# Kernel optimization log

Measured on AMD Instinct MI355X. Metric: run time of the kernel, lower is better.

## Reference

```python
import jax, jax.numpy as jnp
import numpy as np

BAG, SEQ, D = 8, 512, 768      # docs per bag, seq len, bert hidden (d_model)
NB = 4                          # bridge spans kept per doc (subsampling cap regime)
NPD = 2 + NB                    # nodes per doc: h, t, bridges
N = BAG * NPD                   # total entity nodes in the bag graph (48)
T = N * N                       # matrix cells fed to MatTransformer (2304)
H = 8
DK = D // H                     # head dim 96
DFF, L = 1024, 4                # MatTransformer ffn width / num_layers
NREL = 97                       # num_relations (DocRED)
EPS = 1e-5


def _ln(x, g, b):
    m = jnp.mean(x, axis=-1, keepdims=True)
    v = jnp.var(x, axis=-1, keepdims=True)
    return (x - m) * jax.lax.rsqrt(v + EPS) * g + b


def setup_inputs() -> dict:
    key = jax.random.key(0)
    ks = jax.random.split(key, 16)
    s = 0.02
    p = {}
    # stand-in for BERT last hidden states
    p['embedding'] = jax.random.normal(ks[0], (BAG, SEQ, D), jnp.float32)
    # entity spans per doc: [h, t, b1..bNB] x (start, end) inclusive, from get_htb markers
    starts = jax.random.randint(ks[1], (BAG, NPD), 0, SEQ - 9)
    lens = jax.random.randint(ks[2], (BAG, NPD), 1, 9)
    p['spans'] = jnp.stack([starts, starts + lens - 1], axis=-1).astype(jnp.int32)
    # pairwise relation encoders wu / wv / ln1
    p['Wu'] = jax.random.normal(ks[3], (D, D)) * s; p['bu'] = jnp.zeros((D,))
    p['Wv'] = jax.random.normal(ks[4], (D, D)) * s; p['bv'] = jnp.zeros((D,))
    p['Wl'] = jax.random.normal(ks[5], (D, D)) * s; p['bl'] = jnp.zeros((D,))
    # MatTransformer: L layers of MHA + FFN, params stacked over layers
    p['Wq'] = jax.random.normal(ks[6], (L, D, D)) * s;  p['bq'] = jnp.zeros((L, D))
    p['Wk'] = jax.random.normal(ks[7], (L, D, D)) * s;  p['bk'] = jnp.zeros((L, D))
    p['Wvm'] = jax.random.normal(ks[8], (L, D, D)) * s; p['bvm'] = jnp.zeros((L, D))
    p['Wo'] = jax.random.normal(ks[9], (L, D, D)) * s;  p['bo'] = jnp.zeros((L, D))
    p['F1'] = jax.random.normal(ks[10], (L, D, DFF)) * s; p['f1'] = jnp.zeros((L, DFF))
    p['F2'] = jax.random.normal(ks[11], (L, DFF, D)) * s; p['f2'] = jnp.zeros((L, D))
    p['g1'] = jnp.ones((L, D)); p['be1'] = jnp.zeros((L, D))
    p['g2'] = jnp.ones((L, D)); p['be2'] = jnp.zeros((L, D))
    # final norm + predictor
    p['ng'] = jnp.ones((D,)); p['nb'] = jnp.zeros((D,))
    p['Wp'] = jax.random.normal(ks[12], (D, NREL)) * s; p['bp'] = jnp.zeros((NREL,))
    return p


def _forward(embedding, spans, Wu, bu, Wv, bv, Wl, bl, Wq, bq, Wk, bk, Wvm, bvm,
             Wo, bo, F1, f1, F2, f2, g1, be1, g2, be2, ng, nb, Wp, bp):
    # --- ragged span gather + max pooling (masked max, vectorized) ---
    pos = jnp.arange(SEQ)
    m = (pos >= spans[..., :1]) & (pos <= spans[..., 1:])          # [BAG, NPD, SEQ]
    neg = jnp.finfo(embedding.dtype).min
    pooled = jnp.max(jnp.where(m[..., None], embedding[:, None, :, :], neg), axis=2)  # [BAG, NPD, D]
    htb = pooled.reshape(N, D)                                      # h/t/bridge node embs
    # --- pairwise outer-sum relation encoding: relu(ln1(relu(u_i + v_j))) ---
    u = htb @ Wu + bu
    v = htb @ Wv + bv
    rel = jax.nn.relu(jax.nn.relu(u[:, None, :] + v[None, :, :]) @ Wl + bl)  # [N, N, D]
    # --- MatTransformer: multi-head self-attention over the N*N matrix cells ---
    x = rel.reshape(T, D)
    scale = 1.0 / np.sqrt(DK).astype(np.float32)
    for l in range(L):
        q = (x @ Wq[l] + bq[l]).reshape(T, H, DK)
        k = (x @ Wk[l] + bk[l]).reshape(T, H, DK)
        vv = (x @ Wvm[l] + bvm[l]).reshape(T, H, DK)
        att = jax.nn.softmax(jnp.einsum('qhd,khd->hqk', q, k) * scale, axis=-1)
        o = jnp.einsum('hqk,khd->qhd', att, vv).reshape(T, D) @ Wo[l] + bo[l]
        x = _ln(x + o, g1[l], be1[l])
        f = jax.nn.relu(x @ F1[l] + f1[l]) @ F2[l] + f2[l]
        x = _ln(x + f, g2[l], be2[l])
    rel_m = x.reshape(N, N, D)
    # --- gather (h_pos, t_pos) cells: h at i*NPD, t at i*NPD+1 ---
    hp = jnp.arange(BAG) * NPD
    t_feature = rel_m[hp, hp + 1]                                   # [BAG, D]
    ht_logits = _ln(t_feature, ng, nb) @ Wp + bp                    # [BAG, NREL]
    bag_logit = jnp.max(ht_logits, axis=0, keepdims=True)           # [1, NREL]
    return bag_logit, ht_logits


def reference(embedding, spans, Wu, bu, Wv, bv, Wl, bl, Wq, bq, Wk, bk, Wvm, bvm,
              Wo, bo, F1, f1, F2, f2, g1, be1, g2, be2, ng, nb, Wp, bp):
    return _forward(embedding, spans, Wu, bu, Wv, bv, Wl, bl, Wq, bq, Wk, bk,
                    Wvm, bvm, Wo, bo, F1, f1, F2, f2, g1, be1, g2, be2, ng, nb, Wp, bp)
```

## Files before the change

kernel.cpp:

```cpp
#include <hip/hip_runtime.h>
#include <hip/hip_bf16.h>

typedef __hip_bfloat16 bf16;
typedef __bf16 bf16x8 __attribute__((ext_vector_type(8)));
typedef float f32x4 __attribute__((ext_vector_type(4)));

#define BAG 8
#define SEQ 512
#define DM 768
#define NPD 6
#define NNODE 48
#define TT 2304
#define NH 8
#define DKH 96
#define DFF 1024
#define NLAYER 4
#define NREL 97
#define SP 6
#define KSPAN (TT / SP)
#define LN_EPS 1e-5f

__device__ __forceinline__ float b2f(const bf16 x) { return __bfloat162float(x); }
__device__ __forceinline__ bf16 f2b(float f) { return __float2bfloat16(f); }
__device__ __forceinline__ unsigned short f2bu(float f) {
    bf16 h = __float2bfloat16(f);
    return *reinterpret_cast<unsigned short*>(&h);
}

__global__ __launch_bounds__(256) void span_pool(const float* __restrict__ emb,
                                                 const int* __restrict__ spans,
                                                 bf16* __restrict__ htb) {
    const int n = blockIdx.x;
    const int b = n / NPD;
    int s0 = spans[n * 2 + 0];
    int s1 = spans[n * 2 + 1];
    s0 = min(max(s0, 0), SEQ - 1);
    s1 = min(max(s1, s0), SEQ - 1);
    const float* base = emb + (size_t)b * SEQ * DM;
    for (int d = threadIdx.x; d < DM; d += 256) {
        float m = -3.0e38f;
        for (int s = s0; s <= s1; ++s) m = fmaxf(m, base[(size_t)s * DM + d]);
        htb[(size_t)n * DM + d] = f2b(m);
    }
}

__global__ __launch_bounds__(256) void prep_wt3(const float* __restrict__ W0,
                                                const float* __restrict__ W1,
                                                const float* __restrict__ W2,
                                                bf16* __restrict__ Wt) {
    __shared__ __align__(16) __bf16 tile[64][72];
    const int z = blockIdx.z;
    const float* W = (z == 0) ? W0 : (z == 1) ? W1 : W2;
    bf16* out = Wt + (size_t)z * DM * DM;
    const int t = threadIdx.x;
    const int k0 = blockIdx.x * 64, n0 = blockIdx.y * 64;
    const int r = t >> 2, cg = (t & 3) * 16;
#pragma unroll
    for (int i = 0; i < 4; ++i) {
        const float4 v = *(const float4*)&W[(size_t)(k0 + r) * DM + n0 + cg + 4 * i];
        tile[r][cg + 4 * i + 0] = (__bf16)v.x;
        tile[r][cg + 4 * i + 1] = (__bf16)v.y;
        tile[r][cg + 4 * i + 2] = (__bf16)v.z;
        tile[r][cg + 4 * i + 3] = (__bf16)v.w;
    }
    __syncthreads();
#pragma unroll
    for (int i = 0; i < 2; ++i) {
        bf16x8 o;
#pragma unroll
        for (int j = 0; j < 8; ++j) o[j] = tile[cg + 8 * i + j][r];
        *(bf16x8*)&out[(size_t)(n0 + r) * DM + k0 + cg + 8 * i] = o;
    }
}

__global__ __launch_bounds__(256) void prep6(const float* __restrict__ Wq,
                                             const float* __restrict__ Wk,
                                             const float* __restrict__ Wv,
                                             const float* __restrict__ Wo,
                                             const float* __restrict__ F1,
                                             const float* __restrict__ F2,
                                             bf16* __restrict__ slab) {
    __shared__ __align__(16) __bf16 tile[64][72];
    const int z = blockIdx.z;
    int K = DM, N = DM;
    const float* W;
    size_t off;
    switch (z) {
        case 0: W = Wq; off = 0;       break;
        case 1: W = Wk; off = 589824;  break;
        case 2: W = Wv; off = 1179648; break;
        case 3: W = Wo; off = 1769472; break;
        case 4: W = F1; off = 2359296; N = DFF; break;
        default: W = F2; off = 3145728; K = DFF; break;
    }
    const int k0 = blockIdx.x * 64, n0 = blockIdx.y * 64;
    if (k0 >= K || n0 >= N) return;
    bf16* out = slab + off;
    const int t = threadIdx.x;
    const int r = t >> 2, cg = (t & 3) * 16;
#pragma unroll
    for (int i = 0; i < 4; ++i) {
        const float4 v = *(const float4*)&W[(size_t)(k0 + r) * N + n0 + cg + 4 * i];
        tile[r][cg + 4 * i + 0] = (__bf16)v.x;
        tile[r][cg + 4 * i + 1] = (__bf16)v.y;
        tile[r][cg + 4 * i + 2] = (__bf16)v.z;
        tile[r][cg + 4 * i + 3] = (__bf16)v.w;
    }
    __syncthreads();
#pragma unroll
    for (int i = 0; i < 2; ++i) {
        bf16x8 o;
#pragma unroll
        for (int j = 0; j < 8; ++j) o[j] = tile[cg + 8 * i + j][r];
        *(bf16x8*)&out[(size_t)(n0 + r) * K + k0 + cg + 8 * i] = o;
    }
}

template <int RELU, int DUAL>
__global__ __launch_bounds__(256) void gemm_bt256(const bf16* __restrict__ A,
                                                  const bf16* __restrict__ Bt,
                                                  const float* __restrict__ bias,
                                                  const float* __restrict__ bias2,
                                                  bf16* __restrict__ C,
                                                  int M, int N, int K) {
    __shared__ __align__(16) __bf16 As[2][64][72];
    __shared__ __align__(16) __bf16 Bs[2][64][72];
    const int t = threadIdx.x;
    const int w = t >> 6, lane = t & 63;
    const int quad = lane >> 4, l15 = lane & 15;
    const int wr = w >> 1, wc = w & 1;
    const int row0 = blockIdx.y * 64, col0 = blockIdx.x * 64;
    const int s_row = t >> 2, s_off = (t & 3) * 16;
    const bool a_ok = (row0 + s_row) < M;

    const f32x4 fz = {0.f, 0.f, 0.f, 0.f};
    f32x4 acc[2][2];
#pragma unroll
    for (int m = 0; m < 2; ++m)
#pragma unroll
        for (int n = 0; n < 2; ++n) acc[m][n] = fz;

    bf16x8 av[2], bv[2];
#pragma unroll
    for (int j = 0; j < 2; ++j)
#pragma unroll
        for (int e = 0; e < 8; ++e) av[j][e] = (__bf16)0.0f;
    if (a_ok)
#pragma unroll
        for (int j = 0; j < 2; ++j)
            av[j] = *(const bf16x8*)&A[(size_t)(row0 + s_row) * K + s_off + 8 * j];
#pragma unroll
    for (int j = 0; j < 2; ++j)
        bv[j] = *(const bf16x8*)&Bt[(size_t)(col0 + s_row) * K + s_off + 8 * j];

    int cur = 0;
    for (int k0 = 0; k0 < K; k0 += 64) {
#pragma unroll
        for (int j = 0; j < 2; ++j) {
            *(bf16x8*)&As[cur][s_row][s_off + 8 * j] = av[j];
            *(bf16x8*)&Bs[cur][s_row][s_off + 8 * j] = bv[j];
        }
        __syncthreads();

        if (k0 + 64 < K) {
            if (a_ok)
#pragma unroll
                for (int j = 0; j < 2; ++j)
                    av[j] = *(const bf16x8*)&A[(size_t)(row0 + s_row) * K + k0 + 64 + s_off + 8 * j];
#pragma unroll
            for (int j = 0; j < 2; ++j)
                bv[j] = *(const bf16x8*)&Bt[(size_t)(col0 + s_row) * K + k0 + 64 + s_off + 8 * j];
        }

#pragma unroll
        for (int kk = 0; kk < 2; ++kk) {
            const bf16x8 af0 = *(const bf16x8*)&As[cur][wr * 32 + l15][quad * 8 + 32 * kk];
            const bf16x8 af1 = *(const bf16x8*)&As[cur][wr * 32 + 16 + l15][quad * 8 + 32 * kk];
            const bf16x8 bf0 = *(const bf16x8*)&Bs[cur][wc * 32 + l15][quad * 8 + 32 * kk];
            const bf16x8 bf1 = *(const bf16x8*)&Bs[cur][wc * 32 + 16 + l15][quad * 8 + 32 * kk];
            acc[0][0] = __builtin_amdgcn_mfma_f32_16x16x32_bf16(af0, bf0, acc[0][0], 0, 0, 0);
            acc[0][1] = __builtin_amdgcn_mfma_f32_16x16x32_bf16(af0, bf1, acc[0][1], 0, 0, 0);
            acc[1][0] = __builtin_amdgcn_mfma_f32_16x16x32_bf16(af1, bf0, acc[1][0], 0, 0, 0);
            acc[1][1] = __builtin_amdgcn_mfma_f32_16x16x32_bf16(af1, bf1, acc[1][1], 0, 0, 0);
        }
        cur ^= 1;
    }

#pragma unroll
    for (int n = 0; n < 2; ++n) {
        const int col = col0 + wc * 32 + 16 * n + l15;
        const float bvl = (DUAL && col >= DM) ? bias2[col - DM] : bias[col];
#pragma unroll
        for (int m = 0; m < 2; ++m)
#pragma unroll
            for (int r = 0; r < 4; ++r) {
                const int row = row0 + wr * 32 + 16 * m + quad * 4 + r;
                if (row < M) {
                    float v = acc[m][n][r] + bvl;
                    if (RELU) v = fmaxf(v, 0.f);
                    C[(size_t)row * N + col] = f2b(v);
                }
            }
    }
}

__global__ __launch_bounds__(256) void gemm_qkv256(const bf16* __restrict__ A,
                                                   const bf16* __restrict__ Bt,
                                                   const float* __restrict__ b0,
                                                   const float* __restrict__ b1,
                                                   const float* __restrict__ b2,
                                                   bf16* __restrict__ C0,
                                                   bf16* __restrict__ C1,
                                                   bf16* __restrict__ Vt) {
    __shared__ __align__(16) __bf16 As[2][64][72];
    __shared__ __align__(16) __bf16 Bs[2][64][72];
    const int t = threadIdx.x;
    const int w = t >> 6, lane = t & 63;
    const int quad = lane >> 4, l15 = lane & 15;
    const int wr = w >> 1, wc = w & 1;
    const int row0 = blockIdx.y * 64, col0 = blockIdx.x * 64;
    const int s_row = t >> 2, s_off = (t & 3) * 16;

    const f32x4 fz = {0.f, 0.f, 0.f, 0.f};
    f32x4 acc[2][2];
#pragma unroll
    for (int m = 0; m < 2; ++m)
#pragma unroll
        for (int n = 0; n < 2; ++n) acc[m][n] = fz;

    bf16x8 av[2], bv[2];
#pragma unroll
    for (int j = 0; j < 2; ++j) {
        av[j] = *(const bf16x8*)&A[(size_t)(row0 + s_row) * DM + s_off + 8 * j];
        bv[j] = *(const bf16x8*)&Bt[(size_t)(col0 + s_row) * DM + s_off + 8 * j];
    }

    int cur = 0;
    for (int k0 = 0; k0 < DM; k0 += 64) {
#pragma unroll
        for (int j = 0; j < 2; ++j) {
            *(bf16x8*)&As[cur][s_row][s_off + 8 * j] = av[j];
            *(bf16x8*)&Bs[cur][s_row][s_off + 8 * j] = bv[j];
        }
        __syncthreads();

        if (k0 + 64 < DM) {
#pragma unroll
            for (int j = 0; j < 2; ++j) {
                av[j] = *(const bf16x8*)&A[(size_t)(row0 + s_row) * DM + k0 + 64 + s_off + 8 * j];
                bv[j] = *(const bf16x8*)&Bt[(size_t)(col0 + s_row) * DM + k0 + 64 + s_off + 8 * j];
            }
        }

#pragma unroll
        for (int kk = 0; kk < 2; ++kk) {
            const bf16x8 af0 = *(const bf16x8*)&As[cur][wr * 32 + l15][quad * 8 + 32 * kk];
            const bf16x8 af1 = *(const bf16x8*)&As[cur][wr * 32 + 16 + l15][quad * 8 + 32 * kk];
            const bf16x8 bf0 = *(const bf16x8*)&Bs[cur][wc * 32 + l15][quad * 8 + 32 * kk];
            const bf16x8 bf1 = *(const bf16x8*)&Bs[cur][wc * 32 + 16 + l15][quad * 8 + 32 * kk];
            acc[0][0] = __builtin_amdgcn_mfma_f32_16x16x32_bf16(af0, bf0, acc[0][0], 0, 0, 0);
            acc[0][1] = __builtin_amdgcn_mfma_f32_16x16x32_bf16(af0, bf1, acc[0][1], 0, 0, 0);
            acc[1][0] = __builtin_amdgcn_mfma_f32_16x16x32_bf16(af1, bf0, acc[1][0], 0, 0, 0);
            acc[1][1] = __builtin_amdgcn_mfma_f32_16x16x32_bf16(af1, bf1, acc[1][1], 0, 0, 0);
        }
        cur ^= 1;
    }

    const int buf = col0 / DM;
    const int lc0 = col0 - buf * DM;
    if (buf < 2) {
        bf16* Cb = (buf == 0) ? C0 : C1;
        const float* bb = (buf == 0) ? b0 : b1;
#pragma unroll
        for (int n = 0; n < 2; ++n) {
            const int col = lc0 + wc * 32 + 16 * n + l15;
            const float bvl = bb[col];
#pragma unroll
            for (int m = 0; m < 2; ++m)
#pragma unroll
                for (int r = 0; r < 4; ++r) {
                    const int row = row0 + wr * 32 + 16 * m + quad * 4 + r;
                    Cb[(size_t)row * DM + col] = f2b(acc[m][n][r] + bvl);
                }
        }
    } else {
        __bf16 (*Tb)[72] = As[0];
        __syncthreads();
#pragma unroll
        for (int n = 0; n < 2; ++n) {
            const int cl = wc * 32 + 16 * n + l15;
            const float bvl = b2[lc0 + cl];
#pragma unroll
            for (int m = 0; m < 2; ++m)
#pragma unroll
                for (int r = 0; r < 4; ++r)
                    Tb[cl][wr * 32 + 16 * m + quad * 4 + r] = (__bf16)(acc[m][n][r] + bvl);
        }
        __syncthreads();
        const int c = t >> 2, seg = (t & 3) * 16;
        const bf16x8 o0 = *(const bf16x8*)&Tb[c][seg];
        const bf16x8 o1 = *(const bf16x8*)&Tb[c][seg + 8];
        *(bf16x8*)&Vt[(size_t)(lc0 + c) * TT + row0 + seg] = o0;
        *(bf16x8*)&Vt[(size_t)(lc0 + c) * TT + row0 + seg + 8] = o1;
    }
}

template <int RELU>
__global__ __launch_bounds__(128) void gemm_mfma(const bf16* __restrict__ A,
                                                 const float* __restrict__ W,
                                                 const float* __restrict__ bias,
                                                 bf16* __restrict__ C,
                                                 int M, int N, int K) {
    __shared__ __align__(16) __bf16 As[32][40];
    __shared__ __align__(16) __bf16 Bs[64][40];
    const int t = threadIdx.x;
    const int w = t >> 6, lane = t & 63;
    const int quad = lane >> 4, l15 = lane & 15;
    const int row0 = blockIdx.y * 32, col0 = blockIdx.x * 64;
    const int s_row = t >> 2, s_kg = (t & 3) * 8;
    const int s_colg = (t & 15) * 4, s_kp = t >> 4;
    const bool a_ok = (row0 + s_row) < M;
    const f32x4 fz = {0.f, 0.f, 0.f, 0.f};
    f32x4 acc[4];
#pragma unroll
    for (int i = 0; i < 4; ++i) acc[i] = fz;

    for (int k0 = 0; k0 < K; k0 += 32) {
        bf16x8 av;
        for (int j = 0; j < 8; ++j) av[j] = (__bf16)0.0f;
        if (a_ok) av = *(const bf16x8*)&A[(size_t)(row0 + s_row) * K + k0 + s_kg];
        *(bf16x8*)&As[s_row][s_kg] = av;
#pragma unroll
        for (int rep = 0; rep < 2; ++rep) {
            const int kp = s_kp + 8 * rep;
            const size_t gb = (size_t)(k0 + 2 * kp) * N + col0 + s_colg;
            const float4 w0 = *(const float4*)&W[gb];
            const float4 w1 = *(const float4*)&W[gb + N];
#pragma unroll
            for (int i = 0; i < 4; ++i) {
                ushort2 pk;
                pk.x = f2bu((&w0.x)[i]);
                pk.y = f2bu((&w1.x)[i]);
                *(ushort2*)&Bs[s_colg + i][2 * kp] = pk;
            }
        }
        __syncthreads();
        const bf16x8 af = *(const bf16x8*)&As[16 * w + l15][quad * 8];
#pragma unroll
        for (int nt = 0; nt < 4; ++nt) {
            const bf16x8 bfv = *(const bf16x8*)&Bs[16 * nt + l15][quad * 8];
            acc[nt] = __builtin_amdgcn_mfma_f32_16x16x32_bf16(af, bfv, acc[nt], 0, 0, 0);
        }
        __syncthreads();
    }
#pragma unroll
    for (int nt = 0; nt < 4; ++nt) {
        const int col = col0 + 16 * nt + l15;
        const float bvl = bias[col];
#pragma unroll
        for (int r = 0; r < 4; ++r) {
            const int row = row0 + 16 * w + quad * 4 + r;
            if (row < M) {
                float v = acc[nt][r] + bvl;
                if (RELU) v = fmaxf(v, 0.f);
                C[(size_t)row * N + col] = f2b(v);
            }
        }
    }
}

__global__ __launch_bounds__(256) void build_relA(const bf16* __restrict__ u,
                                                  const bf16* __restrict__ v,
                                                  int stride,
                                                  bf16* __restrict__ A) {
    const int cell = blockIdx.x;
    const int i = cell / NNODE, j = cell % NNODE;
    for (int k = threadIdx.x; k < DM; k += 256) {
        A[(size_t)cell * DM + k] =
            f2b(fmaxf(b2f(u[(size_t)i * stride + k]) + b2f(v[(size_t)j * stride + k]), 0.f));
    }
}

__global__ __launch_bounds__(256) void transpose_v(const bf16* __restrict__ v,
                                                   bf16* __restrict__ vt) {
    __shared__ __align__(16) __bf16 tile[64][72];
    const int t = threadIdx.x;
    const int bx = blockIdx.x, by = blockIdx.y;
    const int r = t >> 2, cg = (t & 3) * 16;
#pragma unroll
    for (int i = 0; i < 2; ++i)
        *(bf16x8*)&tile[r][cg + 8 * i] =
            *(const bf16x8*)&v[(size_t)(by * 64 + r) * DM + bx * 64 + cg + 8 * i];
    __syncthreads();
#pragma unroll
    for (int i = 0; i < 2; ++i) {
        bf16x8 o;
#pragma unroll
        for (int j = 0; j < 8; ++j) o[j] = tile[cg + 8 * i + j][r];
        *(bf16x8*)&vt[(size_t)(bx * 64 + r) * TT + by * 64 + cg + 8 * i] = o;
    }
}

template <int MODE>
__global__ __launch_bounds__(256) void attn_mfma(const bf16* __restrict__ qb,
                                                 const bf16* __restrict__ kb,
                                                 const bf16* __restrict__ vtb,
                                                 bf16* __restrict__ ob,
                                                 bf16* __restrict__ Opb,
                                                 float* __restrict__ Lp,
                                                 int kspan) {
    __shared__ __align__(16) __bf16 Ks[64][104];
    __shared__ __align__(16) __bf16 Vts[96][72];
    __shared__ __align__(16) __bf16 Ps[4][16][72];

    const int t = threadIdx.x;
    const int w = t >> 6, lane = t & 63;
    const int quad = lane >> 4, l15 = lane & 15;
    const int h = blockIdx.y;
    const int q0 = blockIdx.x * 64;
    const int p = blockIdx.z;
    const int kstart = p * kspan;
    const float scale = 0.10206207261596575f;

    bf16x8 qf[3];
#pragma unroll
    for (int ks = 0; ks < 3; ++ks) {
        qf[ks] = *(const bf16x8*)&qb[(size_t)(q0 + 16 * w + l15) * DM + h * DKH + quad * 8 + 32 * ks];
#pragma unroll
        for (int j = 0; j < 8; ++j) qf[ks][j] = (__bf16)((float)qf[ks][j] * scale);
    }

    const f32x4 fz = {0.f, 0.f, 0.f, 0.f};
    f32x4 Oa[6];
#pragma unroll
    for (int i = 0; i < 6; ++i) Oa[i] = fz;
    float lrow[4] = {0.f, 0.f, 0.f, 0.f};

    bf16x8 kreg[3], vreg[3];
#pragma unroll
    for (int i = 0; i < 3; ++i) {
        const int idx = t + 256 * i;
        const int r = idx / 12, c = idx % 12;
        kreg[i] = *(const bf16x8*)&kb[(size_t)(kstart + r) * DM + h * DKH + c * 8];
        const int d = idx >> 3, ck = idx & 7;
        vreg[i] = *(const bf16x8*)&vtb[(size_t)(h * DKH + d) * TT + kstart + ck * 8];
    }

    for (int kc = kstart; kc < kstart + kspan; kc += 64) {
        __syncthreads();
#pragma unroll
        for (int i = 0; i < 3; ++i) {
            const int idx = t + 256 * i;
            const int r = idx / 12, c = idx % 12;
            *(bf16x8*)&Ks[r][c * 8] = kreg[i];
            const int d = idx >> 3, ck = idx & 7;
            *(bf16x8*)&Vts[d][ck * 8] = vreg[i];
        }
        __syncthreads();

        if (kc + 64 < kstart + kspan) {
#pragma unroll
            for (int i = 0; i < 3; ++i) {
                const int idx = t + 256 * i;
                const int r = idx / 12, c = idx % 12;
                kreg[i] = *(const bf16x8*)&kb[(size_t)(kc + 64 + r) * DM + h * DKH + c * 8];
                const int d = idx >> 3, ck = idx & 7;
                vreg[i] = *(const bf16x8*)&vtb[(size_t)(h * DKH + d) * TT + kc + 64 + ck * 8];
            }
        }

        f32x4 Sa[4] = {fz, fz, fz, fz};
#pragma unroll
        for (int nt = 0; nt < 4; ++nt)
#pragma unroll
            for (int ks = 0; ks < 3; ++ks) {
                const bf16x8 kf = *(const bf16x8*)&Ks[l15 + 16 * nt][quad * 8 + 32 * ks];
                Sa[nt] = __builtin_amdgcn_mfma_f32_16x16x32_bf16(qf[ks], kf, Sa[nt], 0, 0, 0);
            }

#pragma unroll
        for (int r = 0; r < 4; ++r) {
            const float p0 = __expf(Sa[0][r]), p1 = __expf(Sa[1][r]);
            const float p2 = __expf(Sa[2][r]), p3 = __expf(Sa[3][r]);
            Ps[w][quad * 4 + r][l15]      = (__bf16)p0;
            Ps[w][quad * 4 + r][l15 + 16] = (__bf16)p1;
            Ps[w][quad * 4 + r][l15 + 32] = (__bf16)p2;
            Ps[w][quad * 4 + r][l15 + 48] = (__bf16)p3;
            float ps = p0 + p1 + p2 + p3;
            ps += __shfl_xor(ps, 1);
            ps += __shfl_xor(ps, 2);
            ps += __shfl_xor(ps, 4);
            ps += __shfl_xor(ps, 8);
            lrow[r] += ps;
        }

        const bf16x8 pa0 = *(const bf16x8*)&Ps[w][l15][quad * 8];
        const bf16x8 pa1 = *(const bf16x8*)&Ps[w][l15][32 + quad * 8];

#pragma unroll
        for (int nt = 0; nt < 6; ++nt) {
            const bf16x8 vf0 = *(const bf16x8*)&Vts[l15 + 16 * nt][quad * 8];
            const bf16x8 vf1 = *(const bf16x8*)&Vts[l15 + 16 * nt][32 + quad * 8];
            Oa[nt] = __builtin_amdgcn_mfma_f32_16x16x32_bf16(pa0, vf0, Oa[nt], 0, 0, 0);
            Oa[nt] = __builtin_amdgcn_mfma_f32_16x16x32_bf16(pa1, vf1, Oa[nt], 0, 0, 0);
        }
    }

    if (MODE == 0) {
#pragma unroll
        for (int nt = 0; nt < 6; ++nt)
#pragma unroll
            for (int r = 0; r < 4; ++r) {
                const int row = q0 + 16 * w + quad * 4 + r;
                ob[(size_t)row * DM + h * DKH + 16 * nt + l15] = f2b(Oa[nt][r] / lrow[r]);
            }
    } else {
#pragma unroll
        for (int nt = 0; nt < 6; ++nt)
#pragma unroll
            for (int r = 0; r < 4; ++r) {
                const int row = q0 + 16 * w + quad * 4 + r;
                Opb[((size_t)p * TT + row) * DM + h * DKH + 16 * nt + l15] = f2b(Oa[nt][r]);
            }
        if (l15 == 0) {
#pragma unroll
            for (int r = 0; r < 4; ++r) {
                const int row = q0 + 16 * w + quad * 4 + r;
                Lp[((size_t)p * NH + h) * TT + row] = lrow[r];
            }
        }
    }
}

__global__ __launch_bounds__(256) void attn_merge(const bf16* __restrict__ Opb,
                                                  const float* __restrict__ Lp,
                                                  bf16* __restrict__ ob) {
    __shared__ float Ls[8][NH];
    const int r0 = blockIdx.x * 8;
    const int t = threadIdx.x;
    if (t < 8 * NH) {
        const int rl = t >> 3, hh = t & 7;
        float L = 0.f;
#pragma unroll
        for (int p = 0; p < SP; ++p) L += Lp[((size_t)p * NH + hh) * TT + r0 + rl];
        Ls[rl][hh] = 1.0f / L;
    }
    __syncthreads();
    const int rl = t >> 5, lane = t & 31;
    const int row = r0 + rl;
#pragma unroll
    for (int j = 0; j < 3; ++j) {
        const int d0 = lane * 8 + j * 256;
        float acc[8];
#pragma unroll
        for (int e = 0; e < 8; ++e) acc[e] = 0.f;
#pragma unroll
        for (int p = 0; p < SP; ++p) {
            const bf16x8 vv = *(const bf16x8*)&Opb[((size_t)p * TT + row) * DM + d0];
#pragma unroll
            for (int e = 0; e < 8; ++e) acc[e] += (float)vv[e];
        }
        const float s = Ls[rl][d0 / DKH];
        bf16x8 o;
#pragma unroll
        for (int e = 0; e < 8; ++e) o[e] = (__bf16)(acc[e] * s);
        *(bf16x8*)&ob[(size_t)row * DM + d0] = o;
    }
}

__global__ __launch_bounds__(256) void add_ln(bf16* __restrict__ x,
                                              const bf16* __restrict__ r,
                                              const float* __restrict__ g,
                                              const float* __restrict__ be) {
    __shared__ float red[4];
    const int row = blockIdx.x;
    bf16* xr = x + (size_t)row * DM;
    const bf16* rr = r + (size_t)row * DM;
    const int t = threadIdx.x;

    float v0 = b2f(xr[t]) + b2f(rr[t]);
    float v1 = b2f(xr[t + 256]) + b2f(rr[t + 256]);
    float v2 = b2f(xr[t + 512]) + b2f(rr[t + 512]);
    float s = v0 + v1 + v2;
#pragma unroll
    for (int off = 32; off >= 1; off >>= 1) s += __shfl_xor(s, off);
    if ((t & 63) == 0) red[t >> 6] = s;
    __syncthreads();
    s = red[0] + red[1] + red[2] + red[3];
    const float mean = s * (1.f / 768.f);
    __syncthreads();

    const float d0 = v0 - mean, d1 = v1 - mean, d2 = v2 - mean;
    float ss = d0 * d0 + d1 * d1 + d2 * d2;
#pragma unroll
    for (int off = 32; off >= 1; off >>= 1) ss += __shfl_xor(ss, off);
    if ((t & 63) == 0) red[t >> 6] = ss;
    __syncthreads();
    ss = red[0] + red[1] + red[2] + red[3];
    const float inv = rsqrtf(ss * (1.f / 768.f) + LN_EPS);

    xr[t]       = f2b(d0 * inv * g[t]       + be[t]);
    xr[t + 256] = f2b(d1 * inv * g[t + 256] + be[t + 256]);
    xr[t + 512] = f2b(d2 * inv * g[t + 512] + be[t + 512]);
}

__global__ __launch_bounds__(256) void predict(const bf16* __restrict__ x,
                                               const float* __restrict__ ng,
                                               const float* __restrict__ nb,
                                               const float* __restrict__ Wp,
                                               const float* __restrict__ bp,
                                               float* __restrict__ out) {
    __shared__ float xs[BAG][DM];
    __shared__ float red[4][BAG];
    const int t = threadIdx.x;
    const int rel = blockIdx.x;
    const int wid = t >> 6, lane = t & 63;

    for (int rep = 0; rep < 2; ++rep) {
        const int b = wid + rep * 4;
        const bf16* row = x + (size_t)(294 * b + 1) * DM;
        float vals[12];
        float s = 0.f;
#pragma unroll
        for (int i = 0; i < 12; ++i) { vals[i] = b2f(row[lane + i * 64]); s += vals[i]; }
#pragma unroll
        for (int off = 32; off >= 1; off >>= 1) s += __shfl_xor(s, off);
        const float mean = s * (1.f / 768.f);
        float ss = 0.f;
#pragma unroll
        for (int i = 0; i < 12; ++i) { const float d = vals[i] - mean; ss += d * d; }
#pragma unroll
        for (int off = 32; off >= 1; off >>= 1) ss += __shfl_xor(ss, off);
        const float inv = rsqrtf(ss * (1.f / 768.f) + LN_EPS);
#pragma unroll
        for (int i = 0; i < 12; ++i) {
            const int d = lane + i * 64;
            xs[b][d] = (vals[i] - mean) * inv * ng[d] + nb[d];
        }
    }
    __syncthreads();

    float pb[BAG];
#pragma unroll
    for (int b = 0; b < BAG; ++b) pb[b] = 0.f;
    for (int k = t; k < DM; k += 256) {
        const float wv = Wp[(size_t)k * NREL + rel];
#pragma unroll
        for (int b = 0; b < BAG; ++b) pb[b] += xs[b][k] * wv;
    }
#pragma unroll
    for (int b = 0; b < BAG; ++b)
#pragma unroll
        for (int off = 32; off >= 1; off >>= 1) pb[b] += __shfl_xor(pb[b], off);
    if (lane == 0)
#pragma unroll
        for (int b = 0; b < BAG; ++b) red[wid][b] = pb[b];
    __syncthreads();
    if (t == 0) {
        float mx = -3.0e38f;
        for (int b = 0; b < BAG; ++b) {
            const float v = red[0][b] + red[1][b] + red[2][b] + red[3][b] + bp[rel];
            out[NREL + b * NREL + rel] = v;
            mx = fmaxf(mx, v);
        }
        out[rel] = mx;
    }
}

extern "C" void kernel_launch(void* const* d_in, const int* in_sizes, int n_in,
                              void* d_out, int out_size, void* d_ws, size_t ws_size,
                              hipStream_t stream) {
    const float* emb  = (const float*)d_in[0];
    const int* spans  = (const int*)d_in[1];
    const float* Wu = (const float*)d_in[2];  const float* bu = (const float*)d_in[3];
    const float* Wv = (const float*)d_in[4];  const float* bv = (const float*)d_in[5];
    const float* Wl = (const float*)d_in[6];  const float* bl = (const float*)d_in[7];
    const float* Wq = (const float*)d_in[8];  const float* bq = (const float*)d_in[9];
    const float* Wk = (const float*)d_in[10]; const float* bk = (const float*)d_in[11];
    const float* Wvm = (const float*)d_in[12]; const float* bvm = (const float*)d_in[13];
    const float* Wo = (const float*)d_in[14]; const float* bo = (const float*)d_in[15];
    const float* F1 = (const float*)d_in[16]; const float* f1 = (const float*)d_in[17];
    const float* F2 = (const float*)d_in[18]; const float* f2 = (const float*)d_in[19];
    const float* g1 = (const float*)d_in[20]; const float* be1 = (const float*)d_in[21];
    const float* g2 = (const float*)d_in[22]; const float* be2 = (const float*)d_in[23];
    const float* ng = (const float*)d_in[24]; const float* nb = (const float*)d_in[25];
    const float* Wp = (const float*)d_in[26]; const float* bp = (const float*)d_in[27];

    char* wsb = (char*)d_ws;
    bf16* htb = (bf16*)(wsb + 0);
    bf16* u2  = (bf16*)(wsb + 73728);
    bf16* ub  = (bf16*)(wsb + 73728);
    bf16* vbn = (bf16*)(wsb + 147456);
    bf16* x   = (bf16*)(wsb + 221184);
    bf16* Bq  = (bf16*)(wsb + 3760128);
    bf16* Bk  = (bf16*)(wsb + 7299072);
    bf16* Bv  = (bf16*)(wsb + 10838016);
    bf16* Vt  = (bf16*)(wsb + 15556608);
    bf16* slab = (bf16*)(wsb + 19095552);
    bf16* Opb = (bf16*)(wsb + 26959872);
    float* Lp = (float*)(wsb + 48193536);

    const size_t FULL_END = 48635904;
    const bool use_full = ws_size >= FULL_END;

    span_pool<<<NNODE, 256, 0, stream>>>(emb, spans, htb);

    if (use_full) {
        prep_wt3<<<dim3(12, 12, 3), 256, 0, stream>>>(Wu, Wv, Wl, slab);
        gemm_bt256<0, 1><<<dim3(24, 1), 256, 0, stream>>>(htb, slab, bu, bv, u2,
                                                          NNODE, 2 * DM, DM);
        build_relA<<<TT, 256, 0, stream>>>(u2, u2 + DM, 2 * DM, Bq);
        gemm_bt256<1, 0><<<dim3(12, TT / 64), 256, 0, stream>>>(Bq, slab + 1179648, bl, bl, x,
                                                                TT, DM, DM);

        for (int l = 0; l < NLAYER; ++l) {
            const size_t wo = (size_t)l * DM * DM;
            const size_t f1o = (size_t)l * DM * DFF;
            prep6<<<dim3(16, 16, 6), 256, 0, stream>>>(Wq + wo, Wk + wo, Wvm + wo,
                                                       Wo + wo, F1 + f1o, F2 + f1o, slab);
            gemm_qkv256<<<dim3(36, TT / 64), 256, 0, stream>>>(x, slab, bq + l * DM, bk + l * DM,
                                                               bvm + l * DM, Bq, Bk, Vt);
            attn_mfma<1><<<dim3(TT / 64, NH, SP), 256, 0, stream>>>(Bq, Bk, Vt, Bq, Opb, Lp, KSPAN);
            attn_merge<<<TT / 8, 256, 0, stream>>>(Opb, Lp, Bq);
            gemm_bt256<0, 0><<<dim3(12, TT / 64), 256, 0, stream>>>(Bq, slab + 1769472, bo + l * DM,
                                                                    bo + l * DM, Bk, TT, DM, DM);
            add_ln<<<TT, 256, 0, stream>>>(x, Bk, g1 + l * DM, be1 + l * DM);
            gemm_bt256<1, 0><<<dim3(16, TT / 64), 256, 0, stream>>>(x, slab + 2359296, f1 + l * DFF,
                                                                    f1 + l * DFF, Bv, TT, DFF, DM);
            gemm_bt256<0, 0><<<dim3(12, TT / 64), 256, 0, stream>>>(Bv, slab + 3145728, f2 + l * DM,
                                                                    f2 + l * DM, Bk, TT, DM, DFF);
            add_ln<<<TT, 256, 0, stream>>>(x, Bk, g2 + l * DM, be2 + l * DM);
        }
    } else {
        gemm_mfma<0><<<dim3(12, 2), 128, 0, stream>>>(htb, Wu, bu, ub, NNODE, DM, DM);
        gemm_mfma<0><<<dim3(12, 2), 128, 0, stream>>>(htb, Wv, bv, vbn, NNODE, DM, DM);
        build_relA<<<TT, 256, 0, stream>>>(ub, vbn, DM, Bq);
        gemm_mfma<1><<<dim3(12, TT / 32), 128, 0, stream>>>(Bq, Wl, bl, x, TT, DM, DM);

        for (int l = 0; l < NLAYER; ++l) {
            const size_t wo = (size_t)l * DM * DM;
            const size_t f1o = (size_t)l * DM * DFF;
            gemm_mfma<0><<<dim3(12, TT / 32), 128, 0, stream>>>(x, Wq + wo, bq + l * DM, Bq, TT, DM, DM);
            gemm_mfma<0><<<dim3(12, TT / 32), 128, 0, stream>>>(x, Wk + wo, bk + l * DM, Bk, TT, DM, DM);
            gemm_mfma<0><<<dim3(12, TT / 32), 128, 0, stream>>>(x, Wvm + wo, bvm + l * DM, Bv, TT, DM, DM);
            transpose_v<<<dim3(DM / 64, TT / 64), 256, 0, stream>>>(Bv, Vt);
            attn_mfma<0><<<dim3(TT / 64, NH, 1), 256, 0, stream>>>(Bq, Bk, Vt, Bq, Opb, Lp, TT);
            gemm_mfma<0><<<dim3(12, TT / 32), 128, 0, stream>>>(Bq, Wo + wo, bo + l * DM, Bk, TT, DM, DM);
            add_ln<<<TT, 256, 0, stream>>>(x, Bk, g1 + l * DM, be1 + l * DM);
            gemm_mfma<1><<<dim3(16, TT / 32), 128, 0, stream>>>(x, F1 + f1o, f1 + l * DFF, Bv, TT, DFF, DM);
            gemm_mfma<0><<<dim3(12, TT / 32), 128, 0, stream>>>(Bv, F2 + f1o, f2 + l * DM, Bk, TT, DM, DFF);
            add_ln<<<TT, 256, 0, stream>>>(x, Bk, g2 + l * DM, be2 + l * DM);
        }
    }

    predict<<<NREL, 256, 0, stream>>>(x, ng, nb, Wp, bp, (float*)d_out);
}
```

Measured before the change: 659.6 us.

## Fuse relation build into GEMM, XCD-aware attention blocks, MFMA row sums, exp2

Replaces the separate build_relA pass plus GEMM with a gemm_rel kernel that forms relu(u_i+v_j) on the fly while staging A tiles, avoiding a 2304x768 intermediate write and read. The attention launch becomes 1D, with block IDs remapped so blocks sharing a head and key split land on the same XCD for L2 reuse. Softmax denominators in split mode come from an extra MFMA against a ones row instead of cross-lane shuffles. The exponent switches to exp2 with log2e folded into the scale. The fallback MODE 0 path with 288 blocks gives per = 1, which looks consistent.

```diff
diff --git a/kernel.cpp b/kernel.cpp
--- a/kernel.cpp
+++ b/kernel.cpp
@@ -204,6 +204,87 @@
     }
 }
 
+__global__ __launch_bounds__(256) void gemm_rel(const bf16* __restrict__ u2,
+                                                const bf16* __restrict__ Bt,
+                                                const float* __restrict__ bias,
+                                                bf16* __restrict__ C) {
+    __shared__ __align__(16) __bf16 As[2][64][72];
+    __shared__ __align__(16) __bf16 Bs[2][64][72];
+    const int t = threadIdx.x;
+    const int w = t >> 6, lane = t & 63;
+    const int quad = lane >> 4, l15 = lane & 15;
+    const int wr = w >> 1, wc = w & 1;
+    const int row0 = blockIdx.y * 64, col0 = blockIdx.x * 64;
+    const int s_row = t >> 2, s_off = (t & 3) * 16;
+    const int cell = row0 + s_row;
+    const bf16* up = u2 + (size_t)(cell / NNODE) * (2 * DM);
+    const bf16* vp = u2 + (size_t)(cell % NNODE) * (2 * DM) + DM;
+
+    const f32x4 fz = {0.f, 0.f, 0.f, 0.f};
+    f32x4 acc[2][2];
+#pragma unroll
+    for (int m = 0; m < 2; ++m)
+#pragma unroll
+        for (int n = 0; n < 2; ++n) acc[m][n] = fz;
+
+    bf16x8 uu[2], vv[2], bv[2];
+#pragma unroll
+    for (int j = 0; j < 2; ++j) {
+        uu[j] = *(const bf16x8*)&up[s_off + 8 * j];
+        vv[j] = *(const bf16x8*)&vp[s_off + 8 * j];
+        bv[j] = *(const bf16x8*)&Bt[(size_t)(col0 + s_row) * DM + s_off + 8 * j];
+    }
+
+    int cur = 0;
+    for (int k0 = 0; k0 < DM; k0 += 64) {
+#pragma unroll
+        for (int j = 0; j < 2; ++j) {
+            bf16x8 o;
+#pragma unroll
+            for (int e = 0; e < 8; ++e)
+                o[e] = (__bf16)fmaxf((float)uu[j][e] + (float)vv[j][e], 0.f);
+            *(bf16x8*)&As[cur][s_row][s_off + 8 * j] = o;
+            *(bf16x8*)&Bs[cur][s_row][s_off + 8 * j] = bv[j];
+        }
+        __syncthreads();
+
+        if (k0 + 64 < DM) {
+#pragma unroll
+            for (int j = 0; j < 2; ++j) {
+                uu[j] = *(const bf16x8*)&up[k0 + 64 + s_off + 8 * j];
+                vv[j] = *(const bf16x8*)&vp[k0 + 64 + s_off + 8 * j];
+                bv[j] = *(const bf16x8*)&Bt[(size_t)(col0 + s_row) * DM + k0 + 64 + s_off + 8 * j];
+            }
+        }
+
+#pragma unroll
+        for (int kk = 0; kk < 2; ++kk) {
+            const bf16x8 af0 = *(const bf16x8*)&As[cur][wr * 32 + l15][quad * 8 + 32 * kk];
+            const bf16x8 af1 = *(const bf16x8*)&As[cur][wr * 32 + 16 + l15][quad * 8 + 32 * kk];
+            const bf16x8 bf0 = *(const bf16x8*)&Bs[cur][wc * 32 + l15][quad * 8 + 32 * kk];
+            const bf16x8 bf1 = *(const bf16x8*)&Bs[cur][wc * 32 + 16 + l15][quad * 8 + 32 * kk];
+            acc[0][0] = __builtin_amdgcn_mfma_f32_16x16x32_bf16(af0, bf0, acc[0][0], 0, 0, 0);
+            acc[0][1] = __builtin_amdgcn_mfma_f32_16x16x32_bf16(af0, bf1, acc[0][1], 0, 0, 0);
+            acc[1][0] = __builtin_amdgcn_mfma_f32_16x16x32_bf16(af1, bf0, acc[1][0], 0, 0, 0);
+            acc[1][1] = __builtin_amdgcn_mfma_f32_16x16x32_bf16(af1, bf1, acc[1][1], 0, 0, 0);
+        }
+        cur ^= 1;
+    }
+
+#pragma unroll
+    for (int n = 0; n < 2; ++n) {
+        const int col = col0 + wc * 32 + 16 * n + l15;
+        const float bvl = bias[col];
+#pragma unroll
+        for (int m = 0; m < 2; ++m)
+#pragma unroll
+            for (int r = 0; r < 4; ++r) {
+                const int row = row0 + wr * 32 + 16 * m + quad * 4 + r;
+                C[(size_t)row * DM + col] = f2b(fmaxf(acc[m][n][r] + bvl, 0.f));
+            }
+    }
+}
+
 __global__ __launch_bounds__(256) void gemm_qkv256(const bf16* __restrict__ A,
                                                    const bf16* __restrict__ Bt,
                                                    const float* __restrict__ b0,
@@ -410,17 +491,23 @@
                                                  float* __restrict__ Lp,
                                                  int kspan) {
     __shared__ __align__(16) __bf16 Ks[64][104];
-    __shared__ __align__(16) __bf16 Vts[96][72];
+    __shared__ __align__(16) __bf16 Vts[112][72];
     __shared__ __align__(16) __bf16 Ps[4][16][72];
 
     const int t = threadIdx.x;
     const int w = t >> 6, lane = t & 63;
     const int quad = lane >> 4, l15 = lane & 15;
-    const int h = blockIdx.y;
-    const int q0 = blockIdx.x * 64;
-    const int p = blockIdx.z;
+
+    const int lid = blockIdx.x;
+    const int xcd = lid & 7;
+    const int s = lid >> 3;
+    const int per = gridDim.x / 288;
+    const int combo = xcd * per + s / 36;
+    const int h = combo % NH;
+    const int p = combo / NH;
+    const int q0 = (s % 36) * 64;
     const int kstart = p * kspan;
-    const float scale = 0.10206207261596575f;
+    const float scale = 0.10206207261596575f * 1.4426950408889634f;
 
     bf16x8 qf[3];
 #pragma unroll
@@ -434,7 +521,15 @@
     f32x4 Oa[6];
 #pragma unroll
     for (int i = 0; i < 6; ++i) Oa[i] = fz;
+    f32x4 Lacc = fz;
     float lrow[4] = {0.f, 0.f, 0.f, 0.f};
+
+    if (MODE == 1 && t < 8) {
+        bf16x8 one;
+#pragma unroll
+        for (int e = 0; e < 8; ++e) one[e] = (__bf16)1.0f;
+        *(bf16x8*)&Vts[96][t * 8] = one;
+    }
 
     bf16x8 kreg[3], vreg[3];
 #pragma unroll
@@ -480,18 +575,22 @@
 
 #pragma unroll
         for (int r = 0; r < 4; ++r) {
-            const float p0 = __expf(Sa[0][r]), p1 = __expf(Sa[1][r]);
-            const float p2 = __expf(Sa[2][r]), p3 = __expf(Sa[3][r]);
+            const float p0 = __builtin_amdgcn_exp2f(Sa[0][r]);
+            const float p1 = __builtin_amdgcn_exp2f(Sa[1][r]);
+            const float p2 = __builtin_amdgcn_exp2f(Sa[2][r]);
+            const float p3 = __builtin_amdgcn_exp2f(Sa[3][r]);
             Ps[w][quad * 4 + r][l15]      = (__bf16)p0;
             Ps[w][quad * 4 + r][l15 + 16] = (__bf16)p1;
             Ps[w][quad * 4 + r][l15 + 32] = (__bf16)p2;
             Ps[w][quad * 4 + r][l15 + 48] = (__bf16)p3;
-            float ps = p0 + p1 + p2 + p3;
-            ps += __shfl_xor(ps, 1);
-            ps += __shfl_xor(ps, 2);
-            ps += __shfl_xor(ps, 4);
-            ps += __shfl_xor(ps, 8);
-            lrow[r] += ps;
+            if (MODE == 0) {
+                float ps = p0 + p1 + p2 + p3;
+                ps += __shfl_xor(ps, 1);
+                ps += __shfl_xor(ps, 2);
+                ps += __shfl_xor(ps, 4);
+                ps += __shfl_xor(ps, 8);
+                lrow[r] += ps;
+            }
         }
 
         const bf16x8 pa0 = *(const bf16x8*)&Ps[w][l15][quad * 8];
@@ -504,6 +603,12 @@
             Oa[nt] = __builtin_amdgcn_mfma_f32_16x16x32_bf16(pa0, vf0, Oa[nt], 0, 0, 0);
             Oa[nt] = __builtin_amdgcn_mfma_f32_16x16x32_bf16(pa1, vf1, Oa[nt], 0, 0, 0);
         }
+        if (MODE == 1) {
+            const bf16x8 of0 = *(const bf16x8*)&Vts[96 + l15][quad * 8];
+            const bf16x8 of1 = *(const bf16x8*)&Vts[96 + l15][32 + quad * 8];
+            Lacc = __builtin_amdgcn_mfma_f32_16x16x32_bf16(pa0, of0, Lacc, 0, 0, 0);
+            Lacc = __builtin_amdgcn_mfma_f32_16x16x32_bf16(pa1, of1, Lacc, 0, 0, 0);
+        }
     }
 
     if (MODE == 0) {
@@ -526,7 +631,7 @@
 #pragma unroll
             for (int r = 0; r < 4; ++r) {
                 const int row = q0 + 16 * w + quad * 4 + r;
-                Lp[((size_t)p * NH + h) * TT + row] = lrow[r];
+                Lp[((size_t)p * NH + h) * TT + row] = Lacc[r];
             }
         }
     }
@@ -709,9 +814,7 @@
         prep_wt3<<<dim3(12, 12, 3), 256, 0, stream>>>(Wu, Wv, Wl, slab);
         gemm_bt256<0, 1><<<dim3(24, 1), 256, 0, stream>>>(htb, slab, bu, bv, u2,
                                                           NNODE, 2 * DM, DM);
-        build_relA<<<TT, 256, 0, stream>>>(u2, u2 + DM, 2 * DM, Bq);
-        gemm_bt256<1, 0><<<dim3(12, TT / 64), 256, 0, stream>>>(Bq, slab + 1179648, bl, bl, x,
-                                                                TT, DM, DM);
+        gemm_rel<<<dim3(12, TT / 64), 256, 0, stream>>>(u2, slab + 1179648, bl, x);
 
         for (int l = 0; l < NLAYER; ++l) {
             const size_t wo = (size_t)l * DM * DM;
@@ -720,7 +823,7 @@
                                                        Wo + wo, F1 + f1o, F2 + f1o, slab);
             gemm_qkv256<<<dim3(36, TT / 64), 256, 0, stream>>>(x, slab, bq + l * DM, bk + l * DM,
                                                                bvm + l * DM, Bq, Bk, Vt);
-            attn_mfma<1><<<dim3(TT / 64, NH, SP), 256, 0, stream>>>(Bq, Bk, Vt, Bq, Opb, Lp, KSPAN);
+            attn_mfma<1><<<dim3(36 * NH * SP), 256, 0, stream>>>(Bq, Bk, Vt, Bq, Opb, Lp, KSPAN);
             attn_merge<<<TT / 8, 256, 0, stream>>>(Opb, Lp, Bq);
             gemm_bt256<0, 0><<<dim3(12, TT / 64), 256, 0, stream>>>(Bq, slab + 1769472, bo + l * DM,
                                                                     bo + l * DM, Bk, TT, DM, DM);
@@ -744,7 +847,7 @@
             gemm_mfma<0><<<dim3(12, TT / 32), 128, 0, stream>>>(x, Wk + wo, bk + l * DM, Bk, TT, DM, DM);
             gemm_mfma<0><<<dim3(12, TT / 32), 128, 0, stream>>>(x, Wvm + wo, bvm + l * DM, Bv, TT, DM, DM);
             transpose_v<<<dim3(DM / 64, TT / 64), 256, 0, stream>>>(Bv, Vt);
-            attn_mfma<0><<<dim3(TT / 64, NH, 1), 256, 0, stream>>>(Bq, Bk, Vt, Bq, Opb, Lp, TT);
+            attn_mfma<0><<<dim3(36 * NH), 256, 0, stream>>>(Bq, Bk, Vt, Bq, Opb, Lp, TT);
             gemm_mfma<0><<<dim3(12, TT / 32), 128, 0, stream>>>(Bq, Wo + wo, bo + l * DM, Bk, TT, DM, DM);
             add_ln<<<TT, 256, 0, stream>>>(x, Bk, g1 + l * DM, be1 + l * DM);
             gemm_mfma<1><<<dim3(16, TT / 32), 128, 0, stream>>>(x, F1 + f1o, f1 + l * DFF, Bv, TT, DFF, DM);
```

After: 644.7 us. 2.3% less time.
